# Kernel tuning notes

Measured on AMD Instinct MI355X. Metric: run time of the kernel, lower is better.

The kernel has to match this reference:

```python
import jax, jax.numpy as jnp
import numpy as np

OUT_H, OUT_W, GRID_SIZE = 256, 192, 5
N_CTRL = GRID_SIZE * GRID_SIZE  # 25 control points


def _tps_constants():
    # Control points on a regular grid in [-1, 1]^2 (matches tf.meshgrid order)
    ax = np.linspace(-1.0, 1.0, GRID_SIZE).astype(np.float32)
    P_Y, P_X = np.meshgrid(ax, ax)
    P_X = P_X.reshape(-1).astype(np.float32)  # [N]
    P_Y = P_Y.reshape(-1).astype(np.float32)  # [N]
    # L matrix and its inverse (TPS system)
    d2 = (P_X[:, None] - P_X[None, :]) ** 2 + (P_Y[:, None] - P_Y[None, :]) ** 2
    d2[d2 == 0] = 1.0
    K = d2 * np.log(d2)  # [N, N]
    O = np.ones((N_CTRL, 1), np.float32)
    P = np.concatenate([O, P_X[:, None], P_Y[:, None]], axis=1)  # [N, 3]
    L = np.concatenate([
        np.concatenate([K, P], axis=1),
        np.concatenate([P.T, np.zeros((3, 3), np.float32)], axis=1),
    ], axis=0)  # [N+3, N+3]
    Li = np.linalg.inv(L).astype(np.float32)
    # Output sampling grid in [-1, 1]
    grid_X, grid_Y = np.meshgrid(np.linspace(-1, 1, OUT_W), np.linspace(-1, 1, OUT_H))
    return (jnp.asarray(Li), jnp.asarray(P_X), jnp.asarray(P_Y),
            jnp.asarray(grid_X, dtype=jnp.float32), jnp.asarray(grid_Y, dtype=jnp.float32))

_LI, _PX, _PY, _GX, _GY = _tps_constants()


def setup_inputs() -> dict:
    key = jax.random.key(0)
    theta = jax.random.normal(key, (256, 2 * N_CTRL), dtype=jnp.float32) * 0.1
    return {"theta": theta}


def reference(theta) -> jnp.ndarray:
    # theta: [B, 2N] -> control point displacements
    Q_X = theta[:, :N_CTRL] + _PX  # [B, N]
    Q_Y = theta[:, N_CTRL:] + _PY  # [B, N]
    Li_w = _LI[:N_CTRL, :N_CTRL]   # [N, N]
    Li_a = _LI[N_CTRL:, :N_CTRL]   # [3, N] (rows N..N+2 used; last rows unused by A[:3])
    W_X = jnp.einsum('nm,bm->bn', Li_w, Q_X)  # [B, N] RBF weights
    W_Y = jnp.einsum('nm,bm->bn', Li_w, Q_Y)
    A_X = jnp.einsum('nm,bm->bn', Li_a, Q_X)[:, :3]  # [B, 3] affine part
    A_Y = jnp.einsum('nm,bm->bn', Li_a, Q_Y)[:, :3]
    # RBF kernel U(r) = r^2 log(r^2) between each grid point and each control point
    dX = _GX[:, :, None] - _PX  # [H, W, N]
    dY = _GY[:, :, None] - _PY
    d2 = dX * dX + dY * dY
    d2 = jnp.where(d2 == 0, 1.0, d2)
    U = d2 * jnp.log(d2)  # [H, W, N]
    # Warped coordinates: affine + sum_n W_n * U_n
    px = _GX[None, :, :]  # [1, H, W]
    py = _GY[None, :, :]
    X_prime = (A_X[:, 0, None, None] + A_X[:, 1, None, None] * px
               + A_X[:, 2, None, None] * py + jnp.einsum('hwn,bn->bhw', U, W_X))
    Y_prime = (A_Y[:, 0, None, None] + A_Y[:, 1, None, None] * px
               + A_Y[:, 2, None, None] * py + jnp.einsum('hwn,bn->bhw', U, W_Y))
    return jnp.stack([X_prime, Y_prime], axis=-1)  # [B, H, W, 2]
```

## Files before the change

kernel.cpp:

```cpp
#include <hip/hip_runtime.h>

#define OUT_H 256
#define OUT_W 192
#define NPIX  (OUT_H * OUT_W)
#define NB    256
#define NC    25
#define NL    28
#define BCHUNK 16

typedef float f4_t __attribute__((ext_vector_type(4)));

constexpr double cx_log(double x) {
    int k = 0;
    while (x > 1.5) { x *= 0.5; ++k; }
    while (x < 0.75) { x *= 2.0; --k; }
    double z = (x - 1.0) / (x + 1.0);
    double z2 = z * z;
    double t = z, s = 0.0;
    for (int i = 0; i < 16; ++i) { s += t / (double)(2 * i + 1); t *= z2; }
    return 2.0 * s + (double)k * 0.69314718055994530941723212145817656808;
}

struct LiMat { float v[NL][NC]; };

constexpr LiMat make_li() {
    double aug[NL][2 * NL] = {};
    const double ax[5] = {-1.0, -0.5, 0.0, 0.5, 1.0};
    for (int i = 0; i < NL; ++i)
        for (int j = 0; j < NL; ++j) {
            double v = 0.0;
            if (i < NC && j < NC) {
                double dx = ax[i / 5] - ax[j / 5];
                double dy = ax[i % 5] - ax[j % 5];
                double d2 = dx * dx + dy * dy;
                v = (d2 == 0.0) ? 0.0 : d2 * cx_log(d2);
            } else if (i < NC) {
                v = (j == NC) ? 1.0 : ((j == NC + 1) ? ax[i / 5] : ax[i % 5]);
            } else if (j < NC) {
                v = (i == NC) ? 1.0 : ((i == NC + 1) ? ax[j / 5] : ax[j % 5]);
            }
            aug[i][j] = (double)(float)v;
        }
    for (int i = 0; i < NL; ++i) aug[i][NL + i] = 1.0;

    for (int k = 0; k < NL; ++k) {
        int p = k;
        double best = aug[k][k] < 0 ? -aug[k][k] : aug[k][k];
        for (int r = k + 1; r < NL; ++r) {
            double a = aug[r][k] < 0 ? -aug[r][k] : aug[r][k];
            if (a > best) { best = a; p = r; }
        }
        if (p != k)
            for (int j = k; j < 2 * NL; ++j) {
                double t = aug[k][j]; aug[k][j] = aug[p][j]; aug[p][j] = t;
            }
        const double ipv = 1.0 / aug[k][k];
        for (int j = k; j < 2 * NL; ++j) aug[k][j] *= ipv;
        for (int r = 0; r < NL; ++r) {
            if (r == k) continue;
            const double f = aug[r][k];
            if (f == 0.0) continue;
            for (int j = k; j < 2 * NL; ++j) aug[r][j] -= f * aug[k][j];
        }
    }
    LiMat o = {};
    for (int i = 0; i < NL; ++i)
        for (int j = 0; j < NC; ++j)
            o.v[i][j] = (float)aug[i][NL + j];
    return o;
}

constexpr LiMat LI_HOST = make_li();
__constant__ LiMat LI = LI_HOST;
__constant__ float WC[NB * 64];

__global__ __launch_bounds__(64) void tps_coeff(const float* __restrict__ theta,
                                                float* __restrict__ wc) {
    __shared__ float sth[64 * 2 * NC];
    const int t = threadIdx.x;
    const int gbase = blockIdx.x * 64 * 2 * NC;
    #pragma unroll
    for (int k = 0; k < 2 * NC; ++k) {
        const int idx = k * 64 + t;
        sth[idx] = theta[gbase + idx];
    }
    __syncthreads();

    const float axf[5] = {-1.f, -0.5f, 0.f, 0.5f, 1.f};
    float q[2 * NC];
    #pragma unroll
    for (int m = 0; m < NC; ++m) {
        q[m]      = sth[t * 2 * NC + m]      + axf[m / 5];
        q[NC + m] = sth[t * 2 * NC + NC + m] + axf[m % 5];
    }

    float* wb = wc + ((blockIdx.x * 64 + t) << 6);
    #pragma unroll
    for (int n = 0; n < NL; ++n) {
        float sx = 0.f, sy = 0.f;
        #pragma unroll
        for (int m = 0; m < NC; ++m) {
            const float l = LI.v[n][m];
            sx = fmaf(l, q[m],      sx);
            sy = fmaf(l, q[NC + m], sy);
        }
        if (n < NC) { wb[n] = sx; wb[NC + n] = sy; }
        else        { wb[50 + (n - NC)] = sx; wb[53 + (n - NC)] = sy; }
    }
}

__global__ __launch_bounds__(256) void tps_main(f4_t* __restrict__ out4) {
    const int pp = blockIdx.x * 256 + threadIdx.x;
    const int h  = pp / (OUT_W / 2);
    const int w0 = (pp - h * (OUT_W / 2)) * 2;

    const float gy  = (h == OUT_H - 1) ? 1.f : (float)(-1.0 + h * (2.0 / (OUT_H - 1)));
    const float gx0 = (float)(-1.0 + w0 * (2.0 / (OUT_W - 1)));
    const float gx1 = (w0 + 1 == OUT_W - 1) ? 1.f
                                            : (float)(-1.0 + (w0 + 1) * (2.0 / (OUT_W - 1)));

    const float axf[5] = {-1.f, -0.5f, 0.f, 0.5f, 1.f};
    float U0[NC], U1[NC];
    #pragma unroll
    for (int n = 0; n < NC; ++n) {
        const float cx = axf[n / 5], cy = axf[n % 5];
        const float dy  = gy - cy;
        const float dx0 = gx0 - cx;
        const float d20 = dx0 * dx0 + dy * dy;
        U0[n] = (d20 == 0.f) ? 0.f : d20 * __logf(d20);
        const float dx1 = gx1 - cx;
        const float d21 = dx1 * dx1 + dy * dy;
        U1[n] = (d21 == 0.f) ? 0.f : d21 * __logf(d21);
    }

    const int b0 = blockIdx.y * BCHUNK;
    for (int bi = 0; bi < BCHUNK; ++bi) {
        const int b = b0 + bi;
        const int o = b << 6;
        float X0 = fmaf(WC[o + 52], gy, fmaf(WC[o + 51], gx0, WC[o + 50]));
        float X1 = fmaf(WC[o + 52], gy, fmaf(WC[o + 51], gx1, WC[o + 50]));
        float Y0 = fmaf(WC[o + 55], gy, fmaf(WC[o + 54], gx0, WC[o + 53]));
        float Y1 = fmaf(WC[o + 55], gy, fmaf(WC[o + 54], gx1, WC[o + 53]));
        #pragma unroll
        for (int n = 0; n < NC; ++n) {
            const float wx = WC[o + n];
            const float wy = WC[o + NC + n];
            X0 = fmaf(U0[n], wx, X0);
            X1 = fmaf(U1[n], wx, X1);
            Y0 = fmaf(U0[n], wy, Y0);
            Y1 = fmaf(U1[n], wy, Y1);
        }
        f4_t v; v.x = X0; v.y = Y0; v.z = X1; v.w = Y1;
        out4[(size_t)b * (NPIX / 2) + pp] = v;
    }
}

extern "C" void kernel_launch(void* const* d_in, const int* in_sizes, int n_in,
                              void* d_out, int out_size, void* d_ws, size_t ws_size,
                              hipStream_t stream) {
    const float* theta = (const float*)d_in[0];

    void* wcsym = nullptr;
    hipGetSymbolAddress(&wcsym, HIP_SYMBOL(WC));

    tps_coeff<<<NB / 64, 64, 0, stream>>>(theta, (float*)wcsym);
    dim3 grid(NPIX / 2 / 256, NB / BCHUNK);
    tps_main<<<grid, 256, 0, stream>>>((f4_t*)d_out);
}
```

Baseline: 42.12 us.

## Fuse TPS coefficient solve into main kernel with shared-memory weights

Merges the coefficient kernel into the main warp kernel. Each block recomputes the TPS weights for its 32-batch chunk into shared memory, then reads them with vectorized LDS loads instead of from constant memory. This removes one launch, the hipGetSymbolAddress call and the dependency between the two kernels. BCHUNK is doubled and output stores become nontemporal. In exchange, every pixel block redundantly recomputes the small matrix-vector products.

```diff
diff --git a/kernel.cpp b/kernel.cpp
--- a/kernel.cpp
+++ b/kernel.cpp
@@ -3,10 +3,11 @@
 #define OUT_H 256
 #define OUT_W 192
 #define NPIX  (OUT_H * OUT_W)
+#define NPP   (NPIX / 2)
 #define NB    256
 #define NC    25
 #define NL    28
-#define BCHUNK 16
+#define BCHUNK 32
 
 typedef float f4_t __attribute__((ext_vector_type(4)));
 
@@ -72,45 +73,51 @@
 
 constexpr LiMat LI_HOST = make_li();
 __constant__ LiMat LI = LI_HOST;
-__constant__ float WC[NB * 64];
 
-__global__ __launch_bounds__(64) void tps_coeff(const float* __restrict__ theta,
-                                                float* __restrict__ wc) {
-    __shared__ float sth[64 * 2 * NC];
-    const int t = threadIdx.x;
-    const int gbase = blockIdx.x * 64 * 2 * NC;
+__global__ __launch_bounds__(256) void tps_fused(const float* __restrict__ theta,
+                                                 f4_t* __restrict__ out4) {
+    __shared__ float sth[BCHUNK * 2 * NC];
+    __shared__ float swc[BCHUNK][56];
+
+    const int tid = threadIdx.x;
+    const int b0  = blockIdx.y * BCHUNK;
+
     #pragma unroll
-    for (int k = 0; k < 2 * NC; ++k) {
-        const int idx = k * 64 + t;
-        sth[idx] = theta[gbase + idx];
+    for (int k = 0; k < BCHUNK * 2 * NC; k += 256) {
+        const int idx = k + tid;
+        if (idx < BCHUNK * 2 * NC) sth[idx] = theta[b0 * 2 * NC + idx];
     }
     __syncthreads();
 
     const float axf[5] = {-1.f, -0.5f, 0.f, 0.5f, 1.f};
-    float q[2 * NC];
-    #pragma unroll
-    for (int m = 0; m < NC; ++m) {
-        q[m]      = sth[t * 2 * NC + m]      + axf[m / 5];
-        q[NC + m] = sth[t * 2 * NC + NC + m] + axf[m % 5];
+
+    {
+        const int b = tid >> 3;
+        const int g = tid & 7;
+        if (g < 7) {
+            float qx[NC], qy[NC];
+            #pragma unroll
+            for (int m = 0; m < NC; ++m) {
+                qx[m] = sth[b * 2 * NC + m]      + axf[m / 5];
+                qy[m] = sth[b * 2 * NC + NC + m] + axf[m % 5];
+            }
+            #pragma unroll
+            for (int r = 0; r < 4; ++r) {
+                const int n = g * 4 + r;
+                float sx = 0.f, sy = 0.f;
+                #pragma unroll
+                for (int m = 0; m < NC; ++m) {
+                    const float l = LI.v[n][m];
+                    sx = fmaf(l, qx[m], sx);
+                    sy = fmaf(l, qy[m], sy);
+                }
+                if (n < NC) { swc[b][n] = sx;              swc[b][NC + n] = sy; }
+                else        { swc[b][50 + (n - NC)] = sx;  swc[b][53 + (n - NC)] = sy; }
+            }
+        }
     }
 
-    float* wb = wc + ((blockIdx.x * 64 + t) << 6);
-    #pragma unroll
-    for (int n = 0; n < NL; ++n) {
-        float sx = 0.f, sy = 0.f;
-        #pragma unroll
-        for (int m = 0; m < NC; ++m) {
-            const float l = LI.v[n][m];
-            sx = fmaf(l, q[m],      sx);
-            sy = fmaf(l, q[NC + m], sy);
-        }
-        if (n < NC) { wb[n] = sx; wb[NC + n] = sy; }
-        else        { wb[50 + (n - NC)] = sx; wb[53 + (n - NC)] = sy; }
-    }
-}
-
-__global__ __launch_bounds__(256) void tps_main(f4_t* __restrict__ out4) {
-    const int pp = blockIdx.x * 256 + threadIdx.x;
+    const int pp = blockIdx.x * 256 + tid;
     const int h  = pp / (OUT_W / 2);
     const int w0 = (pp - h * (OUT_W / 2)) * 2;
 
@@ -119,7 +126,6 @@
     const float gx1 = (w0 + 1 == OUT_W - 1) ? 1.f
                                             : (float)(-1.0 + (w0 + 1) * (2.0 / (OUT_W - 1)));
 
-    const float axf[5] = {-1.f, -0.5f, 0.f, 0.5f, 1.f};
     float U0[NC], U1[NC];
     #pragma unroll
     for (int n = 0; n < NC; ++n) {
@@ -133,25 +139,27 @@
         U1[n] = (d21 == 0.f) ? 0.f : d21 * __logf(d21);
     }
 
-    const int b0 = blockIdx.y * BCHUNK;
+    __syncthreads();
+
     for (int bi = 0; bi < BCHUNK; ++bi) {
-        const int b = b0 + bi;
-        const int o = b << 6;
-        float X0 = fmaf(WC[o + 52], gy, fmaf(WC[o + 51], gx0, WC[o + 50]));
-        float X1 = fmaf(WC[o + 52], gy, fmaf(WC[o + 51], gx1, WC[o + 50]));
-        float Y0 = fmaf(WC[o + 55], gy, fmaf(WC[o + 54], gx0, WC[o + 53]));
-        float Y1 = fmaf(WC[o + 55], gy, fmaf(WC[o + 54], gx1, WC[o + 53]));
+        float c[56];
+        #pragma unroll
+        for (int k = 0; k < 14; ++k)
+            *(f4_t*)&c[k * 4] = *(const f4_t*)&swc[bi][k * 4];
+
+        float X0 = fmaf(c[52], gy, fmaf(c[51], gx0, c[50]));
+        float X1 = fmaf(c[52], gy, fmaf(c[51], gx1, c[50]));
+        float Y0 = fmaf(c[55], gy, fmaf(c[54], gx0, c[53]));
+        float Y1 = fmaf(c[55], gy, fmaf(c[54], gx1, c[53]));
         #pragma unroll
         for (int n = 0; n < NC; ++n) {
-            const float wx = WC[o + n];
-            const float wy = WC[o + NC + n];
-            X0 = fmaf(U0[n], wx, X0);
-            X1 = fmaf(U1[n], wx, X1);
-            Y0 = fmaf(U0[n], wy, Y0);
-            Y1 = fmaf(U1[n], wy, Y1);
+            X0 = fmaf(U0[n], c[n],      X0);
+            X1 = fmaf(U1[n], c[n],      X1);
+            Y0 = fmaf(U0[n], c[NC + n], Y0);
+            Y1 = fmaf(U1[n], c[NC + n], Y1);
         }
         f4_t v; v.x = X0; v.y = Y0; v.z = X1; v.w = Y1;
-        out4[(size_t)b * (NPIX / 2) + pp] = v;
+        __builtin_nontemporal_store(v, &out4[(size_t)(b0 + bi) * NPP + pp]);
     }
 }
 
@@ -159,11 +167,6 @@
                               void* d_out, int out_size, void* d_ws, size_t ws_size,
                               hipStream_t stream) {
     const float* theta = (const float*)d_in[0];
-
-    void* wcsym = nullptr;
-    hipGetSymbolAddress(&wcsym, HIP_SYMBOL(WC));
-
-    tps_coeff<<<NB / 64, 64, 0, stream>>>(theta, (float*)wcsym);
-    dim3 grid(NPIX / 2 / 256, NB / BCHUNK);
-    tps_main<<<grid, 256, 0, stream>>>((f4_t*)d_out);
+    dim3 grid(NPP / 256, NB / BCHUNK);
+    tps_fused<<<grid, 256, 0, stream>>>(theta, (f4_t*)d_out);
 }
```

After: 35.73 us. 15.2% less time.
